# Optimization experiments

Measured on AMD Instinct MI355X. Metric: run time of the kernel, lower is better.

The kernel has to match this reference:

```python
import jax, jax.numpy as jnp
import numpy as np

B, N, D, H = 4, 2048, 1024, 16
HD = D // H  # head_dim = 64


def setup_inputs() -> dict:
    key = jax.random.key(0)
    ks = jax.random.split(key, 7)
    q = jax.random.normal(ks[0], (B, N, D), dtype=jnp.float32)
    k = jax.random.normal(ks[1], (B, N, D), dtype=jnp.float32)
    v = jax.random.normal(ks[2], (B, N, D), dtype=jnp.float32)
    scale = 0.02
    Wq = jax.random.normal(ks[3], (D, D), dtype=jnp.float32) * scale
    Wk = jax.random.normal(ks[4], (D, D), dtype=jnp.float32) * scale
    Wv = jax.random.normal(ks[5], (D, D), dtype=jnp.float32) * scale
    Wo = jax.random.normal(ks[6], (D, D), dtype=jnp.float32) * scale
    return {"q": q, "k": k, "v": v, "Wq": Wq, "Wk": Wk, "Wv": Wv, "Wo": Wo}


def _split_heads(x):
    # b n (h d) -> b h n d
    b, n, d = x.shape
    return x.reshape(b, n, H, HD).transpose(0, 2, 1, 3)


def reference(q, k, v, Wq, Wk, Wv, Wo):
    # nn.Linear(bias=False): y = x @ W.T
    qh = _split_heads(q @ Wq.T)
    kh = _split_heads(k @ Wk.T)
    vh = _split_heads(v @ Wv.T)
    scale = jnp.sqrt(jnp.asarray(HD, dtype=jnp.float32))
    scores = jnp.einsum('bhqd,bhkd->bhqk', qh, kh) / scale  # [B,H,N,N]
    # future (causal) mask: triu(ones, diagonal=1) -> masked_fill(-inf)
    future_mask = jnp.triu(jnp.ones((N, N), dtype=bool), k=1)
    scores = jnp.where(future_mask[None, None, :, :], -jnp.inf, scores)
    attn = jax.nn.softmax(scores, axis=-1)
    out = jnp.einsum('bhqk,bhkd->bhqd', attn, vh)
    # b h n d -> b n (h d)
    out = out.transpose(0, 2, 1, 3).reshape(B, N, D)
    return out @ Wo.T
```

## Files before the change

### kernel.cpp

```cpp
#include <hip/hip_runtime.h>
#include <hip/hip_bf16.h>

#define BATCH 4
#define NSEQ 2048
#define DMODEL 1024
#define NHEAD 16
#define HDIM 64

typedef __attribute__((ext_vector_type(8))) short short8;
typedef __attribute__((ext_vector_type(4))) float f32x4;
typedef __attribute__((ext_vector_type(16))) float f32x16;
typedef __attribute__((ext_vector_type(2))) int int2v;
typedef unsigned short ushort_t;

__device__ __forceinline__ ushort_t f2bf(float f) {
    union { float f; unsigned u; } x; x.f = f;
    unsigned r = x.u + 0x7fffu + ((x.u >> 16) & 1u);
    return (ushort_t)(r >> 16);
}

__device__ __forceinline__ unsigned cvt_pk_bf16(float lo, float hi) {
    unsigned r;
    asm("v_cvt_pk_bf16_f32 %0, %1, %2" : "=v"(r) : "v"(lo), "v"(hi));
    return r;
}

#define GLOAD16(gp, lp) __builtin_amdgcn_global_load_lds(                       \
    (const __attribute__((address_space(1))) unsigned*)(const void*)(gp),       \
    (__attribute__((address_space(3))) unsigned*)(void*)(lp), 16, 0, 0)

__global__ __launch_bounds__(256) void cvt_qkv(const float* __restrict__ q,
                                               const float* __restrict__ k,
                                               const float* __restrict__ v,
                                               ushort_t* __restrict__ out) {
    int bid = blockIdx.x;
    int which = bid >> 12;
    int lb = bid & 4095;
    const float* in = (which == 0) ? q : ((which == 1) ? k : v);
    size_t i = ((size_t)lb * 256 + threadIdx.x) * 8;
    float4 f0 = *(const float4*)(in + i);
    float4 f1 = *(const float4*)(in + i + 4);
    short8 o;
    o[0] = f2bf(f0.x); o[1] = f2bf(f0.y); o[2] = f2bf(f0.z); o[3] = f2bf(f0.w);
    o[4] = f2bf(f1.x); o[5] = f2bf(f1.y); o[6] = f2bf(f1.z); o[7] = f2bf(f1.w);
    *(short8*)(out + (size_t)which * 8388608 + i) = o;
}

__global__ __launch_bounds__(256) void cvt_w4(const float* __restrict__ w0,
                                              const float* __restrict__ w1,
                                              const float* __restrict__ w2,
                                              const float* __restrict__ w3,
                                              ushort_t* __restrict__ out) {
    int bid = blockIdx.x;
    int which = bid >> 9;
    int lb = bid & 511;
    const float* in = (which == 0) ? w0 : ((which == 1) ? w1 : ((which == 2) ? w2 : w3));
    size_t i = ((size_t)lb * 256 + threadIdx.x) * 8;
    float4 f0 = *(const float4*)(in + i);
    float4 f1 = *(const float4*)(in + i + 4);
    short8 o;
    o[0] = f2bf(f0.x); o[1] = f2bf(f0.y); o[2] = f2bf(f0.z); o[3] = f2bf(f0.w);
    o[4] = f2bf(f1.x); o[5] = f2bf(f1.y); o[6] = f2bf(f1.z); o[7] = f2bf(f1.w);
    *(short8*)(out + (size_t)which * 1048576 + i) = o;
}

__device__ __forceinline__ void storeC(float* C, size_t idx, float v) { C[idx] = v; }
__device__ __forceinline__ void storeC(ushort_t* C, size_t idx, float v) { C[idx] = f2bf(v); }

template <typename OutT, int LAYOUT>
__global__ __launch_bounds__(512) void gemm_bt8(const ushort_t* __restrict__ A,
                                                const ushort_t* __restrict__ Bt,
                                                OutT* __restrict__ C,
                                                int M, int N, int K, float alpha) {
    __shared__ ushort_t As[3][256 * 64];
    __shared__ ushort_t Bs[3][128 * 64];

    int tid = threadIdx.x;
    int l = tid & 63, w = tid >> 6;
    int wm = w >> 1, wn = w & 1;
    int lr = l & 15, lk = l >> 4;

    int bid = blockIdx.x;
    int wg = (bid & 7) * 32 + (bid >> 3);
    int nbc = N >> 7;
    int brow = (wg / nbc) << 8;
    int bcol = (wg % nbc) << 7;

    int srow8 = l >> 3;
    int sx = ((l & 7) ^ srow8) * 8;
    const ushort_t* pAsrc = A + (size_t)(brow + w * 32 + srow8) * K + sx;
    const ushort_t* pBsrc = Bt + (size_t)(bcol + w * 16 + srow8) * K + sx;
    const size_t rowK8 = (size_t)8 * K;

    int colx = (lk << 4) ^ ((lr & 7) << 4);
    int abyte = (wm * 64 + lr) * 128 + colx;
    int bbyte = (wn * 64 + lr) * 128 + colx;

    f32x4 acc[4][4] = {};
    const int NT = K >> 6;

#pragma unroll
    for (int c = 0; c < 4; c++) GLOAD16(pAsrc + c * rowK8,      &As[0][(w * 32 + 8 * c) * 64]);
#pragma unroll
    for (int c = 0; c < 2; c++) GLOAD16(pBsrc + c * rowK8,      &Bs[0][(w * 16 + 8 * c) * 64]);
#pragma unroll
    for (int c = 0; c < 4; c++) GLOAD16(pAsrc + c * rowK8 + 64, &As[1][(w * 32 + 8 * c) * 64]);
#pragma unroll
    for (int c = 0; c < 2; c++) GLOAD16(pBsrc + c * rowK8 + 64, &Bs[1][(w * 16 + 8 * c) * 64]);

    int slot = 0, stslot = 2;
    for (int T = 0; T < NT; ++T) {
        if (T < NT - 1) { asm volatile("s_waitcnt vmcnt(6)" ::: "memory"); }
        else            { asm volatile("s_waitcnt vmcnt(0)" ::: "memory"); }
        __builtin_amdgcn_sched_barrier(0);
        __builtin_amdgcn_s_barrier();
        asm volatile("" ::: "memory");

        const char* ab = (const char*)&As[slot][0];
        const char* bb = (const char*)&Bs[slot][0];
        bool stage = (T + 2 < NT);
        int k2 = (T + 2) << 6;

        short8 af[4], bf_[4];
#pragma unroll
        for (int m = 0; m < 4; m++) af[m]  = *(const short8*)(ab + abyte + m * 2048);
#pragma unroll
        for (int n = 0; n < 4; n++) bf_[n] = *(const short8*)(bb + bbyte + n * 2048);
        if (stage) {
            GLOAD16(pAsrc + 0 * rowK8 + k2, &As[stslot][(w * 32 + 0) * 64]);
            GLOAD16(pAsrc + 1 * rowK8 + k2, &As[stslot][(w * 32 + 8) * 64]);
            GLOAD16(pAsrc + 2 * rowK8 + k2, &As[stslot][(w * 32 + 16) * 64]);
        }
        __builtin_amdgcn_s_setprio(1);
#pragma unroll
        for (int m = 0; m < 4; m++)
#pragma unroll
            for (int n = 0; n < 4; n++)
                acc[m][n] = __builtin_amdgcn_mfma_f32_16x16x32_bf16(af[m], bf_[n], acc[m][n], 0, 0, 0);
        __builtin_amdgcn_s_setprio(0);

#pragma unroll
        for (int m = 0; m < 4; m++) af[m]  = *(const short8*)(ab + (abyte ^ 64) + m * 2048);
#pragma unroll
        for (int n = 0; n < 4; n++) bf_[n] = *(const short8*)(bb + (bbyte ^ 64) + n * 2048);
        if (stage) {
            GLOAD16(pAsrc + 3 * rowK8 + k2, &As[stslot][(w * 32 + 24) * 64]);
            GLOAD16(pBsrc + 0 * rowK8 + k2, &Bs[stslot][(w * 16 + 0) * 64]);
            GLOAD16(pBsrc + 1 * rowK8 + k2, &Bs[stslot][(w * 16 + 8) * 64]);
        }
        __builtin_amdgcn_s_setprio(1);
#pragma unroll
        for (int m = 0; m < 4; m++)
#pragma unroll
            for (int n = 0; n < 4; n++)
                acc[m][n] = __builtin_amdgcn_mfma_f32_16x16x32_bf16(af[m], bf_[n], acc[m][n], 0, 0, 0);
        __builtin_amdgcn_s_setprio(0);

        slot = (slot == 2) ? 0 : slot + 1;
        stslot = (stslot == 2) ? 0 : stslot + 1;
    }

#pragma unroll
    for (int m = 0; m < 4; m++)
#pragma unroll
        for (int n = 0; n < 4; n++)
#pragma unroll
            for (int r = 0; r < 4; r++) {
                int row = brow + wm * 64 + m * 16 + lk * 4 + r;
                int col = bcol + wn * 64 + n * 16 + lr;
                float v = acc[m][n][r] * alpha;
                if (LAYOUT == 0) {
                    storeC(C, (size_t)row * N + col, v);
                } else if (LAYOUT == 1) {
                    int b = row >> 11, nn = row & 2047, h = col >> 6, d = col & 63;
                    size_t idx = ((size_t)(b * NHEAD + h) << 17) + ((size_t)(nn >> 5) << 11) +
                                 ((d >> 4) << 9) + ((nn & 31) << 4) + (d & 15);
                    storeC(C, idx, v);
                } else {
                    int b = row >> 11, kk = row & 2047, h = col >> 6, d = col & 63;
                    size_t idx = ((size_t)(b * NHEAD + h) << 17) + ((size_t)(kk >> 6) << 12) +
                                 ((d >> 5) << 11) + (((kk >> 4) & 3) << 9) + ((d & 31) << 4) + (kk & 15);
                    storeC(C, idx, v);
                }
            }
}

__global__ __launch_bounds__(256, 2) void attn_kernel(const ushort_t* __restrict__ Qp,
                                                      const ushort_t* __restrict__ Kp,
                                                      const ushort_t* __restrict__ VT,
                                                      ushort_t* __restrict__ AO) {
    int tid = threadIdx.x;
    int l = tid & 63, w = tid >> 6;
    int lq = l & 31;
    int hi = l >> 5;
    int p = blockIdx.x * 4 + w;
    int bh = p >> 5;
    int pi = p & 31;
    int qiL = pi, qiH = 63 - pi;
    int jlo = (qiL >> 1) + 1;
    int jhi = (qiH >> 1) + 1;
    int b = bh >> 4;

    const size_t hb = (size_t)bh << 17;
    const size_t base = ((size_t)b * NSEQ) * DMODEL + (size_t)(bh & 15) * HDIM;

    int qgL = qiL * 32 + lq;
    int qgH = qiH * 32 + lq;
    int loff = lq * 16 + 8 * hi;

    short8 qfL[4], qfH[4];
    {
        const ushort_t* qpL = Qp + hb + ((size_t)qiL << 11) + loff;
        const ushort_t* qpH = Qp + hb + ((size_t)qiH << 11) + loff;
#pragma unroll
        for (int c = 0; c < 4; c++) { qfL[c] = *(const short8*)(qpL + (c << 9));
                                      qfH[c] = *(const short8*)(qpH + (c << 9)); }
    }

    f32x16 OL0 = {}, OL1 = {}, OH0 = {}, OH1 = {};
    float lrunL = 0.f, lrunH = 0.f;

    for (int j = 0; j < jhi; ++j) {
        int k0 = j << 6;
        short8 kf0[4], kf1[4], vf0[4], vf1[4];
        {
            const ushort_t* kp = Kp + hb + ((size_t)(2 * j) << 11) + loff;
            const ushort_t* vp = VT + hb + ((size_t)j << 12) + loff;
#pragma unroll
            for (int c = 0; c < 4; c++) {
                kf0[c] = *(const short8*)(kp + (c << 9));
                kf1[c] = *(const short8*)(kp + 2048 + (c << 9));
                vf0[c] = *(const short8*)(vp + (c << 9));
                vf1[c] = *(const short8*)(vp + 2048 + (c << 9));
            }
        }
        {
            f32x16 S0 = {}, S1 = {};
#pragma unroll
            for (int c = 0; c < 4; c++) S0 = __builtin_amdgcn_mfma_f32_32x32x16_bf16(kf0[c], qfH[c], S0, 0, 0, 0);
#pragma unroll
            for (int c = 0; c < 4; c++) S1 = __builtin_amdgcn_mfma_f32_32x32x16_bf16(kf1[c], qfH[c], S1, 0, 0, 0);
            if (j == jhi - 1) {
#pragma unroll
                for (int r = 0; r < 16; r++) {
                    int kk = k0 + (r & 3) + 8 * (r >> 2) + 4 * hi;
                    if (kk > qgH)      S0[r] = -1e30f;
                    if (kk + 32 > qgH) S1[r] = -1e30f;
                }
            }
            float rs0 = 0.f, rs1 = 0.f;
#pragma unroll
            for (int r = 0; r < 16; r++) {
                S0[r] = __builtin_amdgcn_exp2f(S0[r] - 32.f);
                S1[r] = __builtin_amdgcn_exp2f(S1[r] - 32.f);
                rs0 += S0[r]; rs1 += S1[r];
            }
            float rs = rs0 + rs1;
            rs += __shfl_xor(rs, 32);
            lrunH += rs;
            unsigned pw0[8], pw1[8];
#pragma unroll
            for (int jj = 0; jj < 8; jj++) {
                pw0[jj] = cvt_pk_bf16(S0[2 * jj], S0[2 * jj + 1]);
                pw1[jj] = cvt_pk_bf16(S1[2 * jj], S1[2 * jj + 1]);
            }
            short8 pfr[4];
            {
                union U { unsigned u[4]; short8 s; };
                int2v a, bb;
                a  = __builtin_amdgcn_permlane32_swap((int)pw0[0], (int)pw0[2], false, false);
                bb = __builtin_amdgcn_permlane32_swap((int)pw0[1], (int)pw0[3], false, false);
                U u0; u0.u[0] = (unsigned)a[0]; u0.u[1] = (unsigned)bb[0];
                      u0.u[2] = (unsigned)a[1]; u0.u[3] = (unsigned)bb[1];
                pfr[0] = u0.s;
                a  = __builtin_amdgcn_permlane32_swap((int)pw0[4], (int)pw0[6], false, false);
                bb = __builtin_amdgcn_permlane32_swap((int)pw0[5], (int)pw0[7], false, false);
                U u1; u1.u[0] = (unsigned)a[0]; u1.u[1] = (unsigned)bb[0];
                      u1.u[2] = (unsigned)a[1]; u1.u[3] = (unsigned)bb[1];
                pfr[1] = u1.s;
                a  = __builtin_amdgcn_permlane32_swap((int)pw1[0], (int)pw1[2], false, false);
                bb = __builtin_amdgcn_permlane32_swap((int)pw1[1], (int)pw1[3], false, false);
                U u2; u2.u[0] = (unsigned)a[0]; u2.u[1] = (unsigned)bb[0];
                      u2.u[2] = (unsigned)a[1]; u2.u[3] = (unsigned)bb[1];
                pfr[2] = u2.s;
                a  = __builtin_amdgcn_permlane32_swap((int)pw1[4], (int)pw1[6], false, false);
                bb = __builtin_amdgcn_permlane32_swap((int)pw1[5], (int)pw1[7], false, false);
                U u3; u3.u[0] = (unsigned)a[0]; u3.u[1] = (unsigned)bb[0];
                      u3.u[2] = (unsigned)a[1]; u3.u[3] = (unsigned)bb[1];
                pfr[3] = u3.s;
            }
#pragma unroll
            for (int c = 0; c < 4; c++) OH0 = __builtin_amdgcn_mfma_f32_32x32x16_bf16(vf0[c], pfr[c], OH0, 0, 0, 0);
#pragma unroll
            for (int c = 0; c < 4; c++) OH1 = __builtin_amdgcn_mfma_f32_32x32x16_bf16(vf1[c], pfr[c], OH1, 0, 0, 0);
        }
        if (j < jlo) {
            f32x16 S0 = {}, S1 = {};
#pragma unroll
            for (int c = 0; c < 4; c++) S0 = __builtin_amdgcn_mfma_f32_32x32x16_bf16(kf0[c], qfL[c], S0, 0, 0, 0);
#pragma unroll
            for (int c = 0; c < 4; c++) S1 = __builtin_amdgcn_mfma_f32_32x32x16_bf16(kf1[c], qfL[c], S1, 0, 0, 0);
            if (j == jlo - 1) {
#pragma unroll
                for (int r = 0; r < 16; r++) {
                    int kk = k0 + (r & 3) + 8 * (r >> 2) + 4 * hi;
                    if (kk > qgL)      S0[r] = -1e30f;
                    if (kk + 32 > qgL) S1[r] = -1e30f;
                }
            }
            float rs0 = 0.f, rs1 = 0.f;
#pragma unroll
            for (int r = 0; r < 16; r++) {
                S0[r] = __builtin_amdgcn_exp2f(S0[r] - 32.f);
                S1[r] = __builtin_amdgcn_exp2f(S1[r] - 32.f);
                rs0 += S0[r]; rs1 += S1[r];
            }
            float rs = rs0 + rs1;
            rs += __shfl_xor(rs, 32);
            lrunL += rs;
            unsigned pw0[8], pw1[8];
#pragma unroll
            for (int jj = 0; jj < 8; jj++) {
                pw0[jj] = cvt_pk_bf16(S0[2 * jj], S0[2 * jj + 1]);
                pw1[jj] = cvt_pk_bf16(S1[2 * jj], S1[2 * jj + 1]);
            }
            short8 pfr[4];
            {
                union U { unsigned u[4]; short8 s; };
                int2v a, bb;
                a  = __builtin_amdgcn_permlane32_swap((int)pw0[0], (int)pw0[2], false, false);
                bb = __builtin_amdgcn_permlane32_swap((int)pw0[1], (int)pw0[3], false, false);
                U u0; u0.u[0] = (unsigned)a[0]; u0.u[1] = (unsigned)bb[0];
                      u0.u[2] = (unsigned)a[1]; u0.u[3] = (unsigned)bb[1];
                pfr[0] = u0.s;
                a  = __builtin_amdgcn_permlane32_swap((int)pw0[4], (int)pw0[6], false, false);
                bb = __builtin_amdgcn_permlane32_swap((int)pw0[5], (int)pw0[7], false, false);
                U u1; u1.u[0] = (unsigned)a[0]; u1.u[1] = (unsigned)bb[0];
                      u1.u[2] = (unsigned)a[1]; u1.u[3] = (unsigned)bb[1];
                pfr[1] = u1.s;
                a  = __builtin_amdgcn_permlane32_swap((int)pw1[0], (int)pw1[2], false, false);
                bb = __builtin_amdgcn_permlane32_swap((int)pw1[1], (int)pw1[3], false, false);
                U u2; u2.u[0] = (unsigned)a[0]; u2.u[1] = (unsigned)bb[0];
                      u2.u[2] = (unsigned)a[1]; u2.u[3] = (unsigned)bb[1];
                pfr[2] = u2.s;
                a  = __builtin_amdgcn_permlane32_swap((int)pw1[4], (int)pw1[6], false, false);
                bb = __builtin_amdgcn_permlane32_swap((int)pw1[5], (int)pw1[7], false, false);
                U u3; u3.u[0] = (unsigned)a[0]; u3.u[1] = (unsigned)bb[0];
                      u3.u[2] = (unsigned)a[1]; u3.u[3] = (unsigned)bb[1];
                pfr[3] = u3.s;
            }
#pragma unroll
            for (int c = 0; c < 4; c++) OL0 = __builtin_amdgcn_mfma_f32_32x32x16_bf16(vf0[c], pfr[c], OL0, 0, 0, 0);
#pragma unroll
            for (int c = 0; c < 4; c++) OL1 = __builtin_amdgcn_mfma_f32_32x32x16_bf16(vf1[c], pfr[c], OL1, 0, 0, 0);
        }
    }
    {
        float inv = 1.f / lrunL;
        size_t rowoff = base + (size_t)qgL * DMODEL;
#pragma unroll
        for (int q4 = 0; q4 < 4; q4++) {
            uint2 ua = {cvt_pk_bf16(OL0[4 * q4] * inv,     OL0[4 * q4 + 1] * inv),
                        cvt_pk_bf16(OL0[4 * q4 + 2] * inv, OL0[4 * q4 + 3] * inv)};
            *(uint2*)(AO + rowoff + 8 * q4 + 4 * hi) = ua;
            uint2 ub = {cvt_pk_bf16(OL1[4 * q4] * inv,     OL1[4 * q4 + 1] * inv),
                        cvt_pk_bf16(OL1[4 * q4 + 2] * inv, OL1[4 * q4 + 3] * inv)};
            *(uint2*)(AO + rowoff + 32 + 8 * q4 + 4 * hi) = ub;
        }
    }
    {
        float inv = 1.f / lrunH;
        size_t rowoff = base + (size_t)qgH * DMODEL;
#pragma unroll
        for (int q4 = 0; q4 < 4; q4++) {
            uint2 ua = {cvt_pk_bf16(OH0[4 * q4] * inv,     OH0[4 * q4 + 1] * inv),
                        cvt_pk_bf16(OH0[4 * q4 + 2] * inv, OH0[4 * q4 + 3] * inv)};
            *(uint2*)(AO + rowoff + 8 * q4 + 4 * hi) = ua;
            uint2 ub = {cvt_pk_bf16(OH1[4 * q4] * inv,     OH1[4 * q4 + 1] * inv),
                        cvt_pk_bf16(OH1[4 * q4 + 2] * inv, OH1[4 * q4 + 3] * inv)};
            *(uint2*)(AO + rowoff + 32 + 8 * q4 + 4 * hi) = ub;
        }
    }
}

extern "C" void kernel_launch(void* const* d_in, const int* in_sizes, int n_in,
                              void* d_out, int out_size, void* d_ws, size_t ws_size,
                              hipStream_t stream) {
    const float* q  = (const float*)d_in[0];
    const float* k  = (const float*)d_in[1];
    const float* v  = (const float*)d_in[2];
    const float* Wq = (const float*)d_in[3];
    const float* Wk = (const float*)d_in[4];
    const float* Wv = (const float*)d_in[5];
    const float* Wo = (const float*)d_in[6];
    float* out = (float*)d_out;

    const size_t BND = (size_t)BATCH * NSEQ * DMODEL;
    const size_t WSZ = (size_t)DMODEL * DMODEL;
    const size_t need = (7 * BND + 4 * WSZ) * sizeof(ushort_t);
    if (ws_size < need) return;

    ushort_t* ws  = (ushort_t*)d_ws;
    ushort_t* qb  = ws;
    ushort_t* kb  = qb + BND;
    ushort_t* vb  = kb + BND;
    ushort_t* Qp  = vb + BND;
    ushort_t* Kp  = Qp + BND;
    ushort_t* VT  = Kp + BND;
    ushort_t* AO  = VT + BND;
    ushort_t* Wqb = AO + BND;

    const int M = BATCH * NSEQ;

    cvt_qkv<<<3 * 4096, 256, 0, stream>>>(q, k, v, qb);
    cvt_w4<<<4 * 512, 256, 0, stream>>>(Wq, Wk, Wv, Wo, Wqb);

    int gblocks = (M / 256) * (DMODEL / 128);
    gemm_bt8<ushort_t, 1><<<gblocks, 512, 0, stream>>>(qb, Wqb, Qp, M, DMODEL, DMODEL, 0.18033688011112043f);
    gemm_bt8<ushort_t, 1><<<gblocks, 512, 0, stream>>>(kb, Wqb + WSZ, Kp, M, DMODEL, DMODEL, 1.0f);
    gemm_bt8<ushort_t, 2><<<gblocks, 512, 0, stream>>>(vb, Wqb + 2 * WSZ, VT, M, DMODEL, DMODEL, 1.0f);

    attn_kernel<<<512, 256, 0, stream>>>(Qp, Kp, VT, AO);

    gemm_bt8<float, 0><<<256, 512, 0, stream>>>(AO, Wqb + 3 * WSZ, out, M, DMODEL, DMODEL, 1.0f);
}
```

Baseline: 171.2 us.

## Double-buffer K prefetch and interleave high/low query work in attention loop

```diff
diff --git a/kernel.cpp b/kernel.cpp
--- a/kernel.cpp
+++ b/kernel.cpp
@@ -185,6 +185,37 @@
             }
 }
 
+__device__ __forceinline__ void pack_pfr(const f32x16& S0, const f32x16& S1, short8 (&pfr)[4]) {
+    unsigned pw0[8], pw1[8];
+#pragma unroll
+    for (int jj = 0; jj < 8; jj++) {
+        pw0[jj] = cvt_pk_bf16(S0[2 * jj], S0[2 * jj + 1]);
+        pw1[jj] = cvt_pk_bf16(S1[2 * jj], S1[2 * jj + 1]);
+    }
+    union U { unsigned u[4]; short8 s; };
+    int2v a, bb;
+    a  = __builtin_amdgcn_permlane32_swap((int)pw0[0], (int)pw0[2], false, false);
+    bb = __builtin_amdgcn_permlane32_swap((int)pw0[1], (int)pw0[3], false, false);
+    U u0; u0.u[0] = (unsigned)a[0]; u0.u[1] = (unsigned)bb[0];
+          u0.u[2] = (unsigned)a[1]; u0.u[3] = (unsigned)bb[1];
+    pfr[0] = u0.s;
+    a  = __builtin_amdgcn_permlane32_swap((int)pw0[4], (int)pw0[6], false, false);
+    bb = __builtin_amdgcn_permlane32_swap((int)pw0[5], (int)pw0[7], false, false);
+    U u1; u1.u[0] = (unsigned)a[0]; u1.u[1] = (unsigned)bb[0];
+          u1.u[2] = (unsigned)a[1]; u1.u[3] = (unsigned)bb[1];
+    pfr[1] = u1.s;
+    a  = __builtin_amdgcn_permlane32_swap((int)pw1[0], (int)pw1[2], false, false);
+    bb = __builtin_amdgcn_permlane32_swap((int)pw1[1], (int)pw1[3], false, false);
+    U u2; u2.u[0] = (unsigned)a[0]; u2.u[1] = (unsigned)bb[0];
+          u2.u[2] = (unsigned)a[1]; u2.u[3] = (unsigned)bb[1];
+    pfr[2] = u2.s;
+    a  = __builtin_amdgcn_permlane32_swap((int)pw1[4], (int)pw1[6], false, false);
+    bb = __builtin_amdgcn_permlane32_swap((int)pw1[5], (int)pw1[7], false, false);
+    U u3; u3.u[0] = (unsigned)a[0]; u3.u[1] = (unsigned)bb[0];
+          u3.u[2] = (unsigned)a[1]; u3.u[3] = (unsigned)bb[1];
+    pfr[3] = u3.s;
+}
+
 __global__ __launch_bounds__(256, 2) void attn_kernel(const ushort_t* __restrict__ Qp,
                                                       const ushort_t* __restrict__ Kp,
                                                       const ushort_t* __restrict__ VT,
@@ -193,9 +224,10 @@
     int l = tid & 63, w = tid >> 6;
     int lq = l & 31;
     int hi = l >> 5;
-    int p = blockIdx.x * 4 + w;
-    int bh = p >> 5;
-    int pi = p & 31;
+    int bid = blockIdx.x;
+    int x = bid & 7, jj = bid >> 3;
+    int bh = x + 8 * (jj & 7);
+    int pi = (jj >> 3) * 4 + w;
     int qiL = pi, qiH = 63 - pi;
     int jlo = (qiL >> 1) + 1;
     int jhi = (qiH >> 1) + 1;
@@ -208,6 +240,9 @@
     int qgH = qiH * 32 + lq;
     int loff = lq * 16 + 8 * hi;
 
+    const ushort_t* kpbase = Kp + hb + loff;
+    const ushort_t* vpbase = VT + hb + loff;
+
     short8 qfL[4], qfH[4];
     {
         const ushort_t* qpL = Qp + hb + ((size_t)qiL << 11) + loff;
@@ -220,141 +255,100 @@
     f32x16 OL0 = {}, OL1 = {}, OH0 = {}, OH1 = {};
     float lrunL = 0.f, lrunH = 0.f;
 
-    for (int j = 0; j < jhi; ++j) {
-        int k0 = j << 6;
-        short8 kf0[4], kf1[4], vf0[4], vf1[4];
-        {
-            const ushort_t* kp = Kp + hb + ((size_t)(2 * j) << 11) + loff;
-            const ushort_t* vp = VT + hb + ((size_t)j << 12) + loff;
-#pragma unroll
-            for (int c = 0; c < 4; c++) {
-                kf0[c] = *(const short8*)(kp + (c << 9));
-                kf1[c] = *(const short8*)(kp + 2048 + (c << 9));
-                vf0[c] = *(const short8*)(vp + (c << 9));
-                vf1[c] = *(const short8*)(vp + 2048 + (c << 9));
-            }
-        }
-        {
-            f32x16 S0 = {}, S1 = {};
-#pragma unroll
-            for (int c = 0; c < 4; c++) S0 = __builtin_amdgcn_mfma_f32_32x32x16_bf16(kf0[c], qfH[c], S0, 0, 0, 0);
-#pragma unroll
-            for (int c = 0; c < 4; c++) S1 = __builtin_amdgcn_mfma_f32_32x32x16_bf16(kf1[c], qfH[c], S1, 0, 0, 0);
-            if (j == jhi - 1) {
-#pragma unroll
-                for (int r = 0; r < 16; r++) {
-                    int kk = k0 + (r & 3) + 8 * (r >> 2) + 4 * hi;
-                    if (kk > qgH)      S0[r] = -1e30f;
-                    if (kk + 32 > qgH) S1[r] = -1e30f;
-                }
-            }
-            float rs0 = 0.f, rs1 = 0.f;
-#pragma unroll
-            for (int r = 0; r < 16; r++) {
-                S0[r] = __builtin_amdgcn_exp2f(S0[r] - 32.f);
-                S1[r] = __builtin_amdgcn_exp2f(S1[r] - 32.f);
-                rs0 += S0[r]; rs1 += S1[r];
-            }
-            float rs = rs0 + rs1;
-            rs += __shfl_xor(rs, 32);
-            lrunH += rs;
-            unsigned pw0[8], pw1[8];
-#pragma unroll
-            for (int jj = 0; jj < 8; jj++) {
-                pw0[jj] = cvt_pk_bf16(S0[2 * jj], S0[2 * jj + 1]);
-                pw1[jj] = cvt_pk_bf16(S1[2 * jj], S1[2 * jj + 1]);
-            }
-            short8 pfr[4];
-            {
-                union U { unsigned u[4]; short8 s; };
-                int2v a, bb;
-                a  = __builtin_amdgcn_permlane32_swap((int)pw0[0], (int)pw0[2], false, false);
-                bb = __builtin_amdgcn_permlane32_swap((int)pw0[1], (int)pw0[3], false, false);
-                U u0; u0.u[0] = (unsigned)a[0]; u0.u[1] = (unsigned)bb[0];
-                      u0.u[2] = (unsigned)a[1]; u0.u[3] = (unsigned)bb[1];
-                pfr[0] = u0.s;
-                a  = __builtin_amdgcn_permlane32_swap((int)pw0[4], (int)pw0[6], false, false);
-                bb = __builtin_amdgcn_permlane32_swap((int)pw0[5], (int)pw0[7], false, false);
-                U u1; u1.u[0] = (unsigned)a[0]; u1.u[1] = (unsigned)bb[0];
-                      u1.u[2] = (unsigned)a[1]; u1.u[3] = (unsigned)bb[1];
-                pfr[1] = u1.s;
-                a  = __builtin_amdgcn_permlane32_swap((int)pw1[0], (int)pw1[2], false, false);
-                bb = __builtin_amdgcn_permlane32_swap((int)pw1[1], (int)pw1[3], false, false);
-                U u2; u2.u[0] = (unsigned)a[0]; u2.u[1] = (unsigned)bb[0];
-                      u2.u[2] = (unsigned)a[1]; u2.u[3] = (unsigned)bb[1];
-                pfr[2] = u2.s;
-                a  = __builtin_amdgcn_permlane32_swap((int)pw1[4], (int)pw1[6], false, false);
-                bb = __builtin_amdgcn_permlane32_swap((int)pw1[5], (int)pw1[7], false, false);
-                U u3; u3.u[0] = (unsigned)a[0]; u3.u[1] = (unsigned)bb[0];
-                      u3.u[2] = (unsigned)a[1]; u3.u[3] = (unsigned)bb[1];
-                pfr[3] = u3.s;
-            }
-#pragma unroll
-            for (int c = 0; c < 4; c++) OH0 = __builtin_amdgcn_mfma_f32_32x32x16_bf16(vf0[c], pfr[c], OH0, 0, 0, 0);
-#pragma unroll
-            for (int c = 0; c < 4; c++) OH1 = __builtin_amdgcn_mfma_f32_32x32x16_bf16(vf1[c], pfr[c], OH1, 0, 0, 0);
-        }
-        if (j < jlo) {
-            f32x16 S0 = {}, S1 = {};
-#pragma unroll
-            for (int c = 0; c < 4; c++) S0 = __builtin_amdgcn_mfma_f32_32x32x16_bf16(kf0[c], qfL[c], S0, 0, 0, 0);
-#pragma unroll
-            for (int c = 0; c < 4; c++) S1 = __builtin_amdgcn_mfma_f32_32x32x16_bf16(kf1[c], qfL[c], S1, 0, 0, 0);
-            if (j == jlo - 1) {
-#pragma unroll
-                for (int r = 0; r < 16; r++) {
-                    int kk = k0 + (r & 3) + 8 * (r >> 2) + 4 * hi;
-                    if (kk > qgL)      S0[r] = -1e30f;
-                    if (kk + 32 > qgL) S1[r] = -1e30f;
-                }
-            }
-            float rs0 = 0.f, rs1 = 0.f;
-#pragma unroll
-            for (int r = 0; r < 16; r++) {
-                S0[r] = __builtin_amdgcn_exp2f(S0[r] - 32.f);
-                S1[r] = __builtin_amdgcn_exp2f(S1[r] - 32.f);
-                rs0 += S0[r]; rs1 += S1[r];
-            }
-            float rs = rs0 + rs1;
-            rs += __shfl_xor(rs, 32);
-            lrunL += rs;
-            unsigned pw0[8], pw1[8];
-#pragma unroll
-            for (int jj = 0; jj < 8; jj++) {
-                pw0[jj] = cvt_pk_bf16(S0[2 * jj], S0[2 * jj + 1]);
-                pw1[jj] = cvt_pk_bf16(S1[2 * jj], S1[2 * jj + 1]);
-            }
-            short8 pfr[4];
-            {
-                union U { unsigned u[4]; short8 s; };
-                int2v a, bb;
-                a  = __builtin_amdgcn_permlane32_swap((int)pw0[0], (int)pw0[2], false, false);
-                bb = __builtin_amdgcn_permlane32_swap((int)pw0[1], (int)pw0[3], false, false);
-                U u0; u0.u[0] = (unsigned)a[0]; u0.u[1] = (unsigned)bb[0];
-                      u0.u[2] = (unsigned)a[1]; u0.u[3] = (unsigned)bb[1];
-                pfr[0] = u0.s;
-                a  = __builtin_amdgcn_permlane32_swap((int)pw0[4], (int)pw0[6], false, false);
-                bb = __builtin_amdgcn_permlane32_swap((int)pw0[5], (int)pw0[7], false, false);
-                U u1; u1.u[0] = (unsigned)a[0]; u1.u[1] = (unsigned)bb[0];
-                      u1.u[2] = (unsigned)a[1]; u1.u[3] = (unsigned)bb[1];
-                pfr[1] = u1.s;
-                a  = __builtin_amdgcn_permlane32_swap((int)pw1[0], (int)pw1[2], false, false);
-                bb = __builtin_amdgcn_permlane32_swap((int)pw1[1], (int)pw1[3], false, false);
-                U u2; u2.u[0] = (unsigned)a[0]; u2.u[1] = (unsigned)bb[0];
-                      u2.u[2] = (unsigned)a[1]; u2.u[3] = (unsigned)bb[1];
-                pfr[2] = u2.s;
-                a  = __builtin_amdgcn_permlane32_swap((int)pw1[4], (int)pw1[6], false, false);
-                bb = __builtin_amdgcn_permlane32_swap((int)pw1[5], (int)pw1[7], false, false);
-                U u3; u3.u[0] = (unsigned)a[0]; u3.u[1] = (unsigned)bb[0];
-                      u3.u[2] = (unsigned)a[1]; u3.u[3] = (unsigned)bb[1];
-                pfr[3] = u3.s;
-            }
-#pragma unroll
-            for (int c = 0; c < 4; c++) OL0 = __builtin_amdgcn_mfma_f32_32x32x16_bf16(vf0[c], pfr[c], OL0, 0, 0, 0);
-#pragma unroll
-            for (int c = 0; c < 4; c++) OL1 = __builtin_amdgcn_mfma_f32_32x32x16_bf16(vf1[c], pfr[c], OL1, 0, 0, 0);
-        }
-    }
+    short8 kA0[4], kA1[4], kB0[4], kB1[4];
+#pragma unroll
+    for (int c = 0; c < 4; c++) { kA0[c] = *(const short8*)(kpbase + (c << 9));
+                                  kA1[c] = *(const short8*)(kpbase + 2048 + (c << 9)); }
+
+#define ATTN_STEP(kc0, kc1, kn0, kn1, J, PREF) do {                              \
+        int j_ = (J); int k0_ = j_ << 6;                                         \
+        short8 vf0[4], vf1[4];                                                   \
+        { const ushort_t* vp = vpbase + ((size_t)j_ << 12);                      \
+          _Pragma("unroll")                                                      \
+          for (int c = 0; c < 4; c++) { vf0[c] = *(const short8*)(vp + (c << 9));\
+                                        vf1[c] = *(const short8*)(vp + 2048 + (c << 9)); } } \
+                                                   \
+        f32x16 S0 = {}, S1 = {};                                                 \
+        _Pragma("unroll")                                                        \
+        for (int c = 0; c < 4; c++) { S0 = __builtin_amdgcn_mfma_f32_32x32x16_bf16(kc0[c], qfH[c], S0, 0, 0, 0); } \
+        _Pragma("unroll")                                                        \
+        for (int c = 0; c < 4; c++) { S1 = __builtin_amdgcn_mfma_f32_32x32x16_bf16(kc1[c], qfH[c], S1, 0, 0, 0); } \
+        if (j_ == jhi - 1) {                                                     \
+            _Pragma("unroll")                                                    \
+            for (int r = 0; r < 16; r++) {                                       \
+                int kk = k0_ + (r & 3) + 8 * (r >> 2) + 4 * hi;                  \
+                if (kk > qgH)      S0[r] = -1e30f;                               \
+                if (kk + 32 > qgH) S1[r] = -1e30f;                               \
+            }                                                                    \
+        }                                                                        \
+        float rsH = 0.f;                                                         \
+        _Pragma("unroll")                                                        \
+        for (int r = 0; r < 16; r++) {                                           \
+            S0[r] = __builtin_amdgcn_exp2f(S0[r] - 32.f);                        \
+            S1[r] = __builtin_amdgcn_exp2f(S1[r] - 32.f);                        \
+            rsH += S0[r] + S1[r];                                                \
+        }                                                                        \
+        rsH += __shfl_xor(rsH, 32);                                              \
+        lrunH += rsH;                                                            \
+        short8 pfrH[4];                                                          \
+        pack_pfr(S0, S1, pfrH);                                                  \
+                                                      \
+        bool actL = (j_ < jlo);                                                  \
+        if (actL) {                                                              \
+            S0 = (f32x16){}; S1 = (f32x16){};                                    \
+            _Pragma("unroll")                                                    \
+            for (int c = 0; c < 4; c++) { S0 = __builtin_amdgcn_mfma_f32_32x32x16_bf16(kc0[c], qfL[c], S0, 0, 0, 0); } \
+            _Pragma("unroll")                                                    \
+            for (int c = 0; c < 4; c++) { S1 = __builtin_amdgcn_mfma_f32_32x32x16_bf16(kc1[c], qfL[c], S1, 0, 0, 0); } \
+        }                                                                        \
+                                              \
+        if (PREF) {                                                              \
+            const ushort_t* kp = kpbase + ((size_t)(2 * (j_ + 1)) << 11);        \
+            _Pragma("unroll")                                                    \
+            for (int c = 0; c < 4; c++) { kn0[c] = *(const short8*)(kp + (c << 9)); \
+                                          kn1[c] = *(const short8*)(kp + 2048 + (c << 9)); } \
+        }                                                                        \
+                                                                       \
+        _Pragma("unroll")                                                        \
+        for (int c = 0; c < 4; c++) { OH0 = __builtin_amdgcn_mfma_f32_32x32x16_bf16(vf0[c], pfrH[c], OH0, 0, 0, 0); } \
+        _Pragma("unroll")                                                        \
+        for (int c = 0; c < 4; c++) { OH1 = __builtin_amdgcn_mfma_f32_32x32x16_bf16(vf1[c], pfrH[c], OH1, 0, 0, 0); } \
+                                                   \
+        if (actL) {                                                              \
+            if (j_ == jlo - 1) {                                                 \
+                _Pragma("unroll")                                                \
+                for (int r = 0; r < 16; r++) {                                   \
+                    int kk = k0_ + (r & 3) + 8 * (r >> 2) + 4 * hi;              \
+                    if (kk > qgL)      S0[r] = -1e30f;                           \
+                    if (kk + 32 > qgL) S1[r] = -1e30f;                           \
+                }                                                                \
+            }                                                                    \
+            float rsL = 0.f;                                                     \
+            _Pragma("unroll")                                                    \
+            for (int r = 0; r < 16; r++) {                                       \
+                S0[r] = __builtin_amdgcn_exp2f(S0[r] - 32.f);                    \
+                S1[r] = __builtin_amdgcn_exp2f(S1[r] - 32.f);                    \
+                rsL += S0[r] + S1[r];                                            \
+            }                                                                    \
+            rsL += __shfl_xor(rsL, 32);                                          \
+            lrunL += rsL;                                                        \
+            short8 pfrL[4];                                                      \
+            pack_pfr(S0, S1, pfrL);                                              \
+            _Pragma("unroll")                                                    \
+            for (int c = 0; c < 4; c++) { OL0 = __builtin_amdgcn_mfma_f32_32x32x16_bf16(vf0[c], pfrL[c], OL0, 0, 0, 0); } \
+            _Pragma("unroll")                                                    \
+            for (int c = 0; c < 4; c++) { OL1 = __builtin_amdgcn_mfma_f32_32x32x16_bf16(vf1[c], pfrL[c], OL1, 0, 0, 0); } \
+        }                                                                        \
+    } while (0)
+
+    int j = 0;
+    for (; j + 1 < jhi; j += 2) {
+        ATTN_STEP(kA0, kA1, kB0, kB1, j, true);
+        ATTN_STEP(kB0, kB1, kA0, kA1, j + 1, (j + 2 < jhi));
+    }
+    if (j < jhi) ATTN_STEP(kA0, kA1, kB0, kB1, j, false);
+#undef ATTN_STEP
+
     {
         float inv = 1.f / lrunL;
         size_t rowoff = base + (size_t)qgL * DMODEL;
```

New measurement: 168.3 us. Within noise of the previous version (-1.7%).

## Split attention KV loop across wave pairs and merge partials via shared memory

Applied to the files above, without the earlier changes.

```diff
diff --git a/kernel.cpp b/kernel.cpp
--- a/kernel.cpp
+++ b/kernel.cpp
@@ -185,17 +185,54 @@
             }
 }
 
-__global__ __launch_bounds__(256, 2) void attn_kernel(const ushort_t* __restrict__ Qp,
+__device__ __forceinline__ void pack_pfr(const f32x16& S0, const f32x16& S1, short8 (&pfr)[4]) {
+    unsigned pw0[8], pw1[8];
+#pragma unroll
+    for (int jj = 0; jj < 8; jj++) {
+        pw0[jj] = cvt_pk_bf16(S0[2 * jj], S0[2 * jj + 1]);
+        pw1[jj] = cvt_pk_bf16(S1[2 * jj], S1[2 * jj + 1]);
+    }
+    union U { unsigned u[4]; short8 s; };
+    int2v a, bb;
+    a  = __builtin_amdgcn_permlane32_swap((int)pw0[0], (int)pw0[2], false, false);
+    bb = __builtin_amdgcn_permlane32_swap((int)pw0[1], (int)pw0[3], false, false);
+    U u0; u0.u[0] = (unsigned)a[0]; u0.u[1] = (unsigned)bb[0];
+          u0.u[2] = (unsigned)a[1]; u0.u[3] = (unsigned)bb[1];
+    pfr[0] = u0.s;
+    a  = __builtin_amdgcn_permlane32_swap((int)pw0[4], (int)pw0[6], false, false);
+    bb = __builtin_amdgcn_permlane32_swap((int)pw0[5], (int)pw0[7], false, false);
+    U u1; u1.u[0] = (unsigned)a[0]; u1.u[1] = (unsigned)bb[0];
+          u1.u[2] = (unsigned)a[1]; u1.u[3] = (unsigned)bb[1];
+    pfr[1] = u1.s;
+    a  = __builtin_amdgcn_permlane32_swap((int)pw1[0], (int)pw1[2], false, false);
+    bb = __builtin_amdgcn_permlane32_swap((int)pw1[1], (int)pw1[3], false, false);
+    U u2; u2.u[0] = (unsigned)a[0]; u2.u[1] = (unsigned)bb[0];
+          u2.u[2] = (unsigned)a[1]; u2.u[3] = (unsigned)bb[1];
+    pfr[2] = u2.s;
+    a  = __builtin_amdgcn_permlane32_swap((int)pw1[4], (int)pw1[6], false, false);
+    bb = __builtin_amdgcn_permlane32_swap((int)pw1[5], (int)pw1[7], false, false);
+    U u3; u3.u[0] = (unsigned)a[0]; u3.u[1] = (unsigned)bb[0];
+          u3.u[2] = (unsigned)a[1]; u3.u[3] = (unsigned)bb[1];
+    pfr[3] = u3.s;
+}
+
+__global__ __launch_bounds__(256, 3) void attn_kernel(const ushort_t* __restrict__ Qp,
                                                       const ushort_t* __restrict__ Kp,
                                                       const ushort_t* __restrict__ VT,
                                                       ushort_t* __restrict__ AO) {
+    __shared__ float Om[2][64][33];
+    __shared__ float Lm[2][32];
+
     int tid = threadIdx.x;
     int l = tid & 63, w = tid >> 6;
     int lq = l & 31;
     int hi = l >> 5;
-    int p = blockIdx.x * 4 + w;
-    int bh = p >> 5;
-    int pi = p & 31;
+    int bid = blockIdx.x;
+    int x = bid & 7;
+    int bh = x + 8 * ((bid >> 3) & 7);
+    int pg = w >> 1;
+    int sub = w & 1;
+    int pi = ((bid >> 6) << 1) + pg;
     int qiL = pi, qiH = 63 - pi;
     int jlo = (qiL >> 1) + 1;
     int jhi = (qiH >> 1) + 1;
@@ -208,6 +245,9 @@
     int qgH = qiH * 32 + lq;
     int loff = lq * 16 + 8 * hi;
 
+    const ushort_t* kpbase = Kp + hb + loff;
+    const ushort_t* vpbase = VT + hb + loff;
+
     short8 qfL[4], qfH[4];
     {
         const ushort_t* qpL = Qp + hb + ((size_t)qiL << 11) + loff;
@@ -220,12 +260,12 @@
     f32x16 OL0 = {}, OL1 = {}, OH0 = {}, OH1 = {};
     float lrunL = 0.f, lrunH = 0.f;
 
-    for (int j = 0; j < jhi; ++j) {
+    for (int j = sub; j < jhi; j += 2) {
         int k0 = j << 6;
         short8 kf0[4], kf1[4], vf0[4], vf1[4];
         {
-            const ushort_t* kp = Kp + hb + ((size_t)(2 * j) << 11) + loff;
-            const ushort_t* vp = VT + hb + ((size_t)j << 12) + loff;
+            const ushort_t* kp = kpbase + ((size_t)(2 * j) << 11);
+            const ushort_t* vp = vpbase + ((size_t)j << 12);
 #pragma unroll
             for (int c = 0; c < 4; c++) {
                 kf0[c] = *(const short8*)(kp + (c << 9));
@@ -248,47 +288,17 @@
                     if (kk + 32 > qgH) S1[r] = -1e30f;
                 }
             }
-            float rs0 = 0.f, rs1 = 0.f;
+            float rs = 0.f;
 #pragma unroll
             for (int r = 0; r < 16; r++) {
                 S0[r] = __builtin_amdgcn_exp2f(S0[r] - 32.f);
                 S1[r] = __builtin_amdgcn_exp2f(S1[r] - 32.f);
-                rs0 += S0[r]; rs1 += S1[r];
-            }
-            float rs = rs0 + rs1;
+                rs += S0[r] + S1[r];
+            }
             rs += __shfl_xor(rs, 32);
             lrunH += rs;
-            unsigned pw0[8], pw1[8];
-#pragma unroll
-            for (int jj = 0; jj < 8; jj++) {
-                pw0[jj] = cvt_pk_bf16(S0[2 * jj], S0[2 * jj + 1]);
-                pw1[jj] = cvt_pk_bf16(S1[2 * jj], S1[2 * jj + 1]);
-            }
             short8 pfr[4];
-            {
-                union U { unsigned u[4]; short8 s; };
-                int2v a, bb;
-                a  = __builtin_amdgcn_permlane32_swap((int)pw0[0], (int)pw0[2], false, false);
-                bb = __builtin_amdgcn_permlane32_swap((int)pw0[1], (int)pw0[3], false, false);
-                U u0; u0.u[0] = (unsigned)a[0]; u0.u[1] = (unsigned)bb[0];
-                      u0.u[2] = (unsigned)a[1]; u0.u[3] = (unsigned)bb[1];
-                pfr[0] = u0.s;
-                a  = __builtin_amdgcn_permlane32_swap((int)pw0[4], (int)pw0[6], false, false);
-                bb = __builtin_amdgcn_permlane32_swap((int)pw0[5], (int)pw0[7], false, false);
-                U u1; u1.u[0] = (unsigned)a[0]; u1.u[1] = (unsigned)bb[0];
-                      u1.u[2] = (unsigned)a[1]; u1.u[3] = (unsigned)bb[1];
-                pfr[1] = u1.s;
-                a  = __builtin_amdgcn_permlane32_swap((int)pw1[0], (int)pw1[2], false, false);
-                bb = __builtin_amdgcn_permlane32_swap((int)pw1[1], (int)pw1[3], false, false);
-                U u2; u2.u[0] = (unsigned)a[0]; u2.u[1] = (unsigned)bb[0];
-                      u2.u[2] = (unsigned)a[1]; u2.u[3] = (unsigned)bb[1];
-                pfr[2] = u2.s;
-                a  = __builtin_amdgcn_permlane32_swap((int)pw1[4], (int)pw1[6], false, false);
-                bb = __builtin_amdgcn_permlane32_swap((int)pw1[5], (int)pw1[7], false, false);
-                U u3; u3.u[0] = (unsigned)a[0]; u3.u[1] = (unsigned)bb[0];
-                      u3.u[2] = (unsigned)a[1]; u3.u[3] = (unsigned)bb[1];
-                pfr[3] = u3.s;
-            }
+            pack_pfr(S0, S1, pfr);
 #pragma unroll
             for (int c = 0; c < 4; c++) OH0 = __builtin_amdgcn_mfma_f32_32x32x16_bf16(vf0[c], pfr[c], OH0, 0, 0, 0);
 #pragma unroll
@@ -308,76 +318,80 @@
                     if (kk + 32 > qgL) S1[r] = -1e30f;
                 }
             }
-            float rs0 = 0.f, rs1 = 0.f;
+            float rs = 0.f;
 #pragma unroll
             for (int r = 0; r < 16; r++) {
                 S0[r] = __builtin_amdgcn_exp2f(S0[r] - 32.f);
                 S1[r] = __builtin_amdgcn_exp2f(S1[r] - 32.f);
-                rs0 += S0[r]; rs1 += S1[r];
-            }
-            float rs = rs0 + rs1;
+                rs += S0[r] + S1[r];
+            }
             rs += __shfl_xor(rs, 32);
             lrunL += rs;
-            unsigned pw0[8], pw1[8];
-#pragma unroll
-            for (int jj = 0; jj < 8; jj++) {
-                pw0[jj] = cvt_pk_bf16(S0[2 * jj], S0[2 * jj + 1]);
-                pw1[jj] = cvt_pk_bf16(S1[2 * jj], S1[2 * jj + 1]);
-            }
             short8 pfr[4];
-            {
-                union U { unsigned u[4]; short8 s; };
-                int2v a, bb;
-                a  = __builtin_amdgcn_permlane32_swap((int)pw0[0], (int)pw0[2], false, false);
-                bb = __builtin_amdgcn_permlane32_swap((int)pw0[1], (int)pw0[3], false, false);
-                U u0; u0.u[0] = (unsigned)a[0]; u0.u[1] = (unsigned)bb[0];
-                      u0.u[2] = (unsigned)a[1]; u0.u[3] = (unsigned)bb[1];
-                pfr[0] = u0.s;
-                a  = __builtin_amdgcn_permlane32_swap((int)pw0[4], (int)pw0[6], false, false);
-                bb = __builtin_amdgcn_permlane32_swap((int)pw0[5], (int)pw0[7], false, false);
-                U u1; u1.u[0] = (unsigned)a[0]; u1.u[1] = (unsigned)bb[0];
-                      u1.u[2] = (unsigned)a[1]; u1.u[3] = (unsigned)bb[1];
-                pfr[1] = u1.s;
-                a  = __builtin_amdgcn_permlane32_swap((int)pw1[0], (int)pw1[2], false, false);
-                bb = __builtin_amdgcn_permlane32_swap((int)pw1[1], (int)pw1[3], false, false);
-                U u2; u2.u[0] = (unsigned)a[0]; u2.u[1] = (unsigned)bb[0];
-                      u2.u[2] = (unsigned)a[1]; u2.u[3] = (unsigned)bb[1];
-                pfr[2] = u2.s;
-                a  = __builtin_amdgcn_permlane32_swap((int)pw1[4], (int)pw1[6], false, false);
-                bb = __builtin_amdgcn_permlane32_swap((int)pw1[5], (int)pw1[7], false, false);
-                U u3; u3.u[0] = (unsigned)a[0]; u3.u[1] = (unsigned)bb[0];
-                      u3.u[2] = (unsigned)a[1]; u3.u[3] = (unsigned)bb[1];
-                pfr[3] = u3.s;
-            }
+            pack_pfr(S0, S1, pfr);
 #pragma unroll
             for (int c = 0; c < 4; c++) OL0 = __builtin_amdgcn_mfma_f32_32x32x16_bf16(vf0[c], pfr[c], OL0, 0, 0, 0);
 #pragma unroll
             for (int c = 0; c < 4; c++) OL1 = __builtin_amdgcn_mfma_f32_32x32x16_bf16(vf1[c], pfr[c], OL1, 0, 0, 0);
         }
     }
-    {
-        float inv = 1.f / lrunL;
+
+    if (sub == 1) {
+        if (hi == 0) Lm[pg][lq] = lrunH;
+#pragma unroll
+        for (int r = 0; r < 16; r++) {
+            int d0r = (r & 3) + 8 * (r >> 2) + 4 * hi;
+            Om[pg][d0r][lq]      = OH0[r];
+            Om[pg][d0r + 32][lq] = OH1[r];
+        }
+    }
+    __syncthreads();
+    if (sub == 0) {
+        float inv = 1.f / (lrunH + Lm[pg][lq]);
+#pragma unroll
+        for (int r = 0; r < 16; r++) {
+            int d0r = (r & 3) + 8 * (r >> 2) + 4 * hi;
+            OH0[r] = (OH0[r] + Om[pg][d0r][lq]) * inv;
+            OH1[r] = (OH1[r] + Om[pg][d0r + 32][lq]) * inv;
+        }
+        size_t rowoff = base + (size_t)qgH * DMODEL;
+#pragma unroll
+        for (int q4 = 0; q4 < 4; q4++) {
+            uint2 ua = {cvt_pk_bf16(OH0[4 * q4], OH0[4 * q4 + 1]),
+                        cvt_pk_bf16(OH0[4 * q4 + 2], OH0[4 * q4 + 3])};
+            *(uint2*)(AO + rowoff + 8 * q4 + 4 * hi) = ua;
+            uint2 ub = {cvt_pk_bf16(OH1[4 * q4], OH1[4 * q4 + 1]),
+                        cvt_pk_bf16(OH1[4 * q4 + 2], OH1[4 * q4 + 3])};
+            *(uint2*)(AO + rowoff + 32 + 8 * q4 + 4 * hi) = ub;
+        }
+    }
+    __syncthreads();
+    if (sub == 1) {
+        if (hi == 0) Lm[pg][lq] = lrunL;
+#pragma unroll
+        for (int r = 0; r < 16; r++) {
+            int d0r = (r & 3) + 8 * (r >> 2) + 4 * hi;
+            Om[pg][d0r][lq]      = OL0[r];
+            Om[pg][d0r + 32][lq] = OL1[r];
+        }
+    }
+    __syncthreads();
+    if (sub == 0) {
+        float inv = 1.f / (lrunL + Lm[pg][lq]);
+#pragma unroll
+        for (int r = 0; r < 16; r++) {
+            int d0r = (r & 3) + 8 * (r >> 2) + 4 * hi;
+            OL0[r] = (OL0[r] + Om[pg][d0r][lq]) * inv;
+            OL1[r] = (OL1[r] + Om[pg][d0r + 32][lq]) * inv;
+        }
         size_t rowoff = base + (size_t)qgL * DMODEL;
 #pragma unroll
         for (int q4 = 0; q4 < 4; q4++) {
-            uint2 ua = {cvt_pk_bf16(OL0[4 * q4] * inv,     OL0[4 * q4 + 1] * inv),
-                        cvt_pk_bf16(OL0[4 * q4 + 2] * inv, OL0[4 * q4 + 3] * inv)};
+            uint2 ua = {cvt_pk_bf16(OL0[4 * q4], OL0[4 * q4 + 1]),
+                        cvt_pk_bf16(OL0[4 * q4 + 2], OL0[4 * q4 + 3])};
             *(uint2*)(AO + rowoff + 8 * q4 + 4 * hi) = ua;
-            uint2 ub = {cvt_pk_bf16(OL1[4 * q4] * inv,     OL1[4 * q4 + 1] * inv),
-                        cvt_pk_bf16(OL1[4 * q4 + 2] * inv, OL1[4 * q4 + 3] * inv)};
-            *(uint2*)(AO + rowoff + 32 + 8 * q4 + 4 * hi) = ub;
-        }
-    }
-    {
-        float inv = 1.f / lrunH;
-        size_t rowoff = base + (size_t)qgH * DMODEL;
-#pragma unroll
-        for (int q4 = 0; q4 < 4; q4++) {
-            uint2 ua = {cvt_pk_bf16(OH0[4 * q4] * inv,     OH0[4 * q4 + 1] * inv),
-                        cvt_pk_bf16(OH0[4 * q4 + 2] * inv, OH0[4 * q4 + 3] * inv)};
-            *(uint2*)(AO + rowoff + 8 * q4 + 4 * hi) = ua;
-            uint2 ub = {cvt_pk_bf16(OH1[4 * q4] * inv,     OH1[4 * q4 + 1] * inv),
-                        cvt_pk_bf16(OH1[4 * q4 + 2] * inv, OH1[4 * q4 + 3] * inv)};
+            uint2 ub = {cvt_pk_bf16(OL1[4 * q4], OL1[4 * q4 + 1]),
+                        cvt_pk_bf16(OL1[4 * q4 + 2], OL1[4 * q4 + 3])};
             *(uint2*)(AO + rowoff + 32 + 8 * q4 + 4 * hi) = ub;
         }
     }
@@ -420,7 +434,7 @@
     gemm_bt8<ushort_t, 1><<<gblocks, 512, 0, stream>>>(kb, Wqb + WSZ, Kp, M, DMODEL, DMODEL, 1.0f);
     gemm_bt8<ushort_t, 2><<<gblocks, 512, 0, stream>>>(vb, Wqb + 2 * WSZ, VT, M, DMODEL, DMODEL, 1.0f);
 
-    attn_kernel<<<512, 256, 0, stream>>>(Qp, Kp, VT, AO);
-
-    gemm_bt8<float, 0><<<256, 512, 0, stream>>>(AO, Wqb + 3 * WSZ, out, M, DMODEL, DMODEL, 1.0f);
-}
+    attn_kernel<<<1024, 256, 0, stream>>>(Qp, Kp, VT, AO);
+
+    gemm_bt8<float, 0><<<gblocks, 512, 0, stream>>>(AO, Wqb + 3 * WSZ, out, M, DMODEL, DMODEL, 1.0f);
+}
```

New measurement: 305.8 us. +78.6%, slower.
